# Kernel tuning notes

Measured on AMD Instinct MI355X. Metric: run time of the kernel, lower is better.

Reference implementation:

```python
import jax, jax.numpy as jnp
import numpy as np

KH = KW = 9
BN_EPS = 1e-5


def conv3x3(x, w):
    # x: [B,Cin,H,W], w: [Cout,Cin,3,3], stride 1, padding 1
    return jax.lax.conv_general_dilated(
        x, w, window_strides=(1, 1), padding=((1, 1), (1, 1)),
        dimension_numbers=("NCHW", "OIHW", "NCHW"))


def cbr(x, w, bn):
    # bn: [4, C] rows = (gamma, beta, running_mean, running_var); inference-mode BN
    g, b, m, v = bn[0], bn[1], bn[2], bn[3]
    x = conv3x3(x, w)
    x = (x - m[:, None, None]) * (g[:, None, None] / jnp.sqrt(v[:, None, None] + BN_EPS)) + b[:, None, None]
    return jax.nn.relu(x)


def weighting(x, atten):
    # x: [B,C,H,W], atten: [B,H,W,KH*KW]
    # out[b,c,h,w] = sum_k atten[b,h,w,k] * x[b,c, h+dh(k), w+dw(k)]  (zero-padded window)
    B, C, H, W = x.shape
    patches = jax.lax.conv_general_dilated_patches(
        x, filter_shape=(KH, KW), window_strides=(1, 1),
        padding=((KH // 2, KH // 2), (KW // 2, KW // 2)))  # [B, C*KH*KW, H, W], channel-major
    patches = patches.reshape(B, C, KH * KW, H, W)
    return jnp.einsum("bckhw,bhwk->bchw", patches, atten)


def _make_params(key, fc_dim=1024):
    d4, d16 = fc_dim // 4, fc_dim // 16
    ks = jax.random.split(key, 16)
    def conv_w(k, co, ci):
        return jax.random.normal(k, (co, ci, 3, 3), jnp.float32) * (1.0 / np.sqrt(ci * 9))
    def bn(k, c):
        g = 1.0 + 0.1 * jax.random.normal(k, (c,), jnp.float32)
        return jnp.stack([g, jnp.zeros((c,)), jnp.zeros((c,)), jnp.ones((c,))])
    p = {}
    p["w1"], p["bn1"] = conv_w(ks[0], d4, fc_dim), bn(ks[1], d4)
    p["w2"], p["bn2"] = conv_w(ks[2], d16, d4), bn(ks[3], d16)
    p["w3"], p["bn3"] = conv_w(ks[4], d4, d16), bn(ks[5], d4)
    p["w4"], p["bn4"] = conv_w(ks[6], d4, fc_dim), bn(ks[7], d4)
    p["w5"], p["bn5"] = conv_w(ks[8], d4, d4), bn(ks[9], d4)
    p["fw1"] = jax.random.normal(ks[10], (10, d4), jnp.float32) * (1.0 / np.sqrt(d4))
    p["fb1"] = jnp.zeros((10,), jnp.float32)
    p["fw2"] = jax.random.normal(ks[11], (1, 10), jnp.float32) * (1.0 / np.sqrt(10))
    p["fb2"] = jnp.zeros((1,), jnp.float32)
    return p


def setup_inputs() -> dict:
    key = jax.random.key(0)
    k1, k2, k3, kp = jax.random.split(key, 4)
    B, fc_dim, H, W = 4, 1024, 64, 64
    inp = {
        "low_key": jax.random.normal(k1, (B, fc_dim, H, W), jnp.float32),
        "low_nonkey": jax.random.normal(k2, (B, fc_dim, H, W), jnp.float32),
        "local_atten": jax.random.uniform(k3, (B, H, W, KH * KW), jnp.float32),
    }
    inp.update(_make_params(kp, fc_dim))
    return inp


def reference(low_key, low_nonkey, local_atten,
              w1, bn1, w2, bn2, w3, bn3, w4, bn4, w5, bn5,
              fw1, fb1, fw2, fb2):
    x = cbr(low_key, w1, bn1)        # [B, 256, H, W]
    x = cbr(x, w2, bn2)              # [B, 64, H, W]
    x = weighting(x, local_atten)    # 9x9 local-attention weighted gather
    x = cbr(x, w3, bn3)              # [B, 256, H, W]
    y = cbr(low_nonkey, w4, bn4)     # [B, 256, H, W]
    out = cbr(x - y, w5, bn5)        # [B, 256, H, W]
    out = out.mean(axis=(2, 3))      # adaptive avg pool to 1x1 -> [B, 256]
    out = out @ fw1.T + fb1          # [B, 10]
    out = out @ fw2.T + fb2          # [B, 1]
    return out
```

## Files before the change

### kernel.cpp

```cpp
#include <hip/hip_runtime.h>
#include <math.h>

typedef _Float16 f16;
typedef f16 f16x4 __attribute__((ext_vector_type(4)));
typedef f16 f16x8 __attribute__((ext_vector_type(8)));
typedef float f32x4 __attribute__((ext_vector_type(4)));

#define NB 4

__global__ void __launch_bounds__(256)
wtrans_kernel(const float* __restrict__ w, f16* __restrict__ wt, int Co, int Cin) {
  int idx = blockIdx.x * 256 + threadIdx.x;
  int total = Co * Cin * 9;
  if (idx >= total) return;
  int ci = idx % Cin, t2 = idx / Cin;
  int co = t2 % Co, k = t2 / Co;
  wt[idx] = (f16)w[((size_t)co * Cin + ci) * 9 + k];
}

__global__ void __launch_bounds__(256)
nchw2nhwc(const float* __restrict__ in, f16* __restrict__ out) {
  __shared__ f16 s[64][66];
  const int t = threadIdx.x;
  const int bh = blockIdx.x, c0 = blockIdx.y * 64;
  const int b = bh >> 6, h = bh & 63;
  const int w = t & 63, cr = t >> 6;
  #pragma unroll
  for (int i = 0; i < 16; ++i) {
    int c = c0 + cr * 16 + i;
    s[cr * 16 + i][w] = (f16)in[(((size_t)b * 1024 + c) * 64 + h) * 64 + w];
  }
  __syncthreads();
  #pragma unroll
  for (int i = 0; i < 2; ++i) {
    int task = t + 256 * i;
    int oct = task & 7, w2 = task >> 3;
    f16x8 v;
    #pragma unroll
    for (int j = 0; j < 8; ++j) v[j] = s[oct * 8 + j][w2];
    *(f16x8*)(out + (((size_t)b * 64 + h) * 64 + w2) * 1024 + c0 + oct * 8) = v;
  }
}

__global__ void __launch_bounds__(256, 2)
conv_bigK(const f16* __restrict__ in, const f16* __restrict__ wt,
          float* __restrict__ pacc) {
  constexpr int Cin = 1024, Co = 256, NC = 8;
  __shared__ __align__(16) f16 xs[4][66][40];

  const int t = threadIdx.x;
  const int zz = blockIdx.x;
  const int tile = blockIdx.y;
  const int b = tile >> 5;
  const int h0 = (tile & 31) * 2;
  const int ciBase = zz * 256;
  const int wid = t >> 6, lane = t & 63;
  const int l15 = lane & 15, lg = lane >> 4;
  const int koff = lg * 8;

  f32x4 acc[4][8];
  #pragma unroll
  for (int m = 0; m < 4; ++m)
    #pragma unroll
    for (int n = 0; n < 8; ++n)
      #pragma unroll
      for (int r = 0; r < 4; ++r) acc[m][n][r] = 0.f;

  const f16* inb = in + (size_t)b * Cin * 4096;
  const int wS = t >> 2, octS = t & 3;
  f16x8 ireg[4];

  auto load_stage = [&](int c) {
    int ci0 = ciBase + c * 32;
    #pragma unroll
    for (int r = 0; r < 4; ++r) {
      int gh = h0 - 1 + r;
      f16x8 v = {};
      if ((unsigned)gh < 64u)
        v = *(const f16x8*)(inb + ((size_t)gh * 64 + wS) * Cin + ci0 + octS * 8);
      ireg[r] = v;
    }
  };
  auto write_stage = [&]() {
    #pragma unroll
    for (int r = 0; r < 4; ++r)
      *(f16x8*)&xs[r][wS + 1][octS * 8] = ireg[r];
  };

  const f16* wA = wt + (size_t)(wid * 64 + l15) * Cin + koff + ciBase;

  f16x8 af[3][4];
  #pragma unroll
  for (int m = 0; m < 4; ++m) {
    af[0][m] = *(const f16x8*)(wA + (size_t)m * 16 * Cin);
    af[1][m] = *(const f16x8*)(wA + ((size_t)1 * Co + m * 16) * Cin);
  }

  if (t < 32) {
    int r = t >> 3, side = (t >> 2) & 1, oc = t & 3;
    f16x8 z = {};
    *(f16x8*)&xs[r][side * 65][oc * 8] = z;
  }
  load_stage(0);
  write_stage();
  __syncthreads();

  for (int c = 0; c < NC; ++c) {
    if (c + 1 < NC) load_stage(c + 1);
    #pragma unroll
    for (int tap = 0; tap < 9; ++tap) {
      const int dh = tap / 3 - 1, dw = tap % 3 - 1;
      const int pf_tap = (tap < 7) ? tap + 2 : tap - 7;
      const int pf_c = (tap < 7) ? c : c + 1;
      const bool doPf = (tap < 7) || (c + 1 < NC);
      if (doPf)
        #pragma unroll
        for (int m = 0; m < 4; ++m)
          af[(tap + 2) % 3][m] =
              *(const f16x8*)(wA + ((size_t)pf_tap * Co + m * 16) * Cin + pf_c * 32);
      #pragma unroll
      for (int n = 0; n < 8; ++n) {
        const f16x8 bf = *(const f16x8*)&xs[(n >> 2) + dh + 1][(n & 3) * 16 + l15 + 1 + dw][koff];
        #pragma unroll
        for (int m = 0; m < 4; ++m)
          acc[m][n] = __builtin_amdgcn_mfma_f32_16x16x32_f16(af[tap % 3][m], bf, acc[m][n], 0, 0, 0);
      }
    }
    __syncthreads();
    if (c + 1 < NC) write_stage();
    __syncthreads();
  }

  float* pb = pacc + (size_t)zz * 4194304 + (size_t)b * 4096 * Co;
  #pragma unroll
  for (int m = 0; m < 4; ++m)
    #pragma unroll
    for (int n = 0; n < 8; ++n) {
      int px = (h0 + (n >> 2)) * 64 + (n & 3) * 16 + l15;
      *(f32x4*)(pb + (size_t)px * Co + wid * 64 + m * 16 + lg * 4) = acc[m][n];
    }
}

__global__ void __launch_bounds__(256, 1)
conv_mfma(const f16* __restrict__ in, const f16* __restrict__ in2,
          const f16* __restrict__ wt, const float* __restrict__ bn,
          f16* __restrict__ out, float* __restrict__ pacc,
          float* __restrict__ partial, int Cin, int Co, int kspl) {
  __shared__ __align__(16) f16 xs[6][66][40];
  __shared__ __align__(16) f16 ws[9][64][40];
  __shared__ float s_red[4][64];

  const int t = threadIdx.x;
  const int tile = blockIdx.x;
  const int b = tile >> 4;
  const int h0 = (tile & 15) * 4;
  const int co_blk = blockIdx.y * 64;
  const int ciBase = blockIdx.z * (Cin / kspl);
  const int NC = (Cin / kspl) >> 5;
  const int wid = t >> 6, lane = t & 63;
  const int l15 = lane & 15, lg = lane >> 4;
  const int koff = lg * 8;

  f32x4 acc[4][4];
  #pragma unroll
  for (int m = 0; m < 4; ++m)
    #pragma unroll
    for (int n = 0; n < 4; ++n)
      #pragma unroll
      for (int r = 0; r < 4; ++r) acc[m][n][r] = 0.f;

  const f16* inb = in + (size_t)b * Cin * 4096;
  const f16* inb2 = in2 ? in2 + (size_t)b * Cin * 4096 : nullptr;

  const int wS = t >> 2, octS = t & 3;
  f16x8 ireg[6], wreg[9];

  auto load_stage = [&](int ci0) {
    #pragma unroll
    for (int r = 0; r < 6; ++r) {
      int gh = h0 - 1 + r;
      f16x8 v = {};
      if ((unsigned)gh < 64u) {
        size_t off = ((size_t)gh * 64 + wS) * Cin + ci0 + octS * 8;
        v = *(const f16x8*)(inb + off);
        if (inb2) { f16x8 v2 = *(const f16x8*)(inb2 + off); v = v - v2; }
      }
      ireg[r] = v;
    }
    #pragma unroll
    for (int i = 0; i < 9; ++i) {
      int s = t + 256 * i;
      int oct = s & 3, co = (s >> 2) & 63, k = s >> 8;
      wreg[i] = *(const f16x8*)(wt + ((size_t)k * Co + co_blk + co) * Cin + ci0 + oct * 8);
    }
  };
  auto write_stage = [&]() {
    #pragma unroll
    for (int r = 0; r < 6; ++r)
      *(f16x8*)&xs[r][wS + 1][octS * 8] = ireg[r];
    #pragma unroll
    for (int i = 0; i < 9; ++i) {
      int s = t + 256 * i;
      int oct = s & 3, co = (s >> 2) & 63, k = s >> 8;
      *(f16x8*)&ws[k][co][oct * 8] = wreg[i];
    }
  };

  if (t < 48) {
    int r = t >> 3, side = (t >> 2) & 1, oc = t & 3;
    f16x8 z = {};
    *(f16x8*)&xs[r][side * 65][oc * 8] = z;
  }
  load_stage(ciBase);
  write_stage();
  __syncthreads();

  for (int c = 0; c < NC; ++c) {
    if (c + 1 < NC) load_stage(ciBase + ((c + 1) << 5));
    #pragma unroll
    for (int tap = 0; tap < 9; ++tap) {
      const int dh = tap / 3 - 1, dw = tap % 3 - 1;
      f16x8 af[4];
      #pragma unroll
      for (int m = 0; m < 4; ++m)
        af[m] = *(const f16x8*)&ws[tap][m * 16 + l15][koff];
      #pragma unroll
      for (int n = 0; n < 4; ++n) {
        const f16x8 bf = *(const f16x8*)&xs[wid + dh + 1][n * 16 + l15 + 1 + dw][koff];
        #pragma unroll
        for (int m = 0; m < 4; ++m)
          acc[m][n] = __builtin_amdgcn_mfma_f32_16x16x32_f16(af[m], bf, acc[m][n], 0, 0, 0);
      }
    }
    __syncthreads();
    if (c + 1 < NC) write_stage();
    __syncthreads();
  }

  if (pacc) {
    float* pb = pacc + (size_t)blockIdx.z * 16384 * Co + (size_t)b * 4096 * Co;
    #pragma unroll
    for (int m = 0; m < 4; ++m)
      #pragma unroll
      for (int n = 0; n < 4; ++n) {
        int px = (h0 + wid) * 64 + n * 16 + l15;
        *(f32x4*)(pb + (size_t)px * Co + co_blk + m * 16 + lg * 4) = acc[m][n];
      }
  } else if (out) {
    #pragma unroll
    for (int m = 0; m < 4; ++m) {
      float sc[4], sh[4];
      #pragma unroll
      for (int reg = 0; reg < 4; ++reg) {
        int co = co_blk + m * 16 + lg * 4 + reg;
        sc[reg] = bn[co] / sqrtf(bn[3 * Co + co] + 1e-5f);
        sh[reg] = bn[Co + co] - bn[2 * Co + co] * sc[reg];
      }
      #pragma unroll
      for (int n = 0; n < 4; ++n) {
        f16x4 v;
        #pragma unroll
        for (int reg = 0; reg < 4; ++reg)
          v[reg] = (f16)fmaxf(fmaf(acc[m][n][reg], sc[reg], sh[reg]), 0.f);
        *(f16x4*)(out + ((size_t)(b * 64 + h0 + wid) * 64 + n * 16 + l15) * Co
                      + co_blk + m * 16 + lg * 4) = v;
      }
    }
  } else {
    #pragma unroll
    for (int m = 0; m < 4; ++m)
      #pragma unroll
      for (int reg = 0; reg < 4; ++reg) {
        int co = co_blk + m * 16 + lg * 4 + reg;
        float sc = bn[co] / sqrtf(bn[3 * Co + co] + 1e-5f);
        float sh = bn[Co + co] - bn[2 * Co + co] * sc;
        float s = 0.f;
        #pragma unroll
        for (int n = 0; n < 4; ++n)
          s += fmaxf(fmaf(acc[m][n][reg], sc, sh), 0.f);
        s += __shfl_xor(s, 1, 64);
        s += __shfl_xor(s, 2, 64);
        s += __shfl_xor(s, 4, 64);
        s += __shfl_xor(s, 8, 64);
        if (l15 == 0) s_red[wid][m * 16 + lg * 4 + reg] = s;
      }
    __syncthreads();
    if (t < 64) {
      float v = s_red[0][t] + s_red[1][t] + s_red[2][t] + s_red[3][t];
      partial[((size_t)b * Co + co_blk + t) * 16 + (tile & 15)] = v;
    }
  }
}

__global__ void __launch_bounds__(256)
kreduce(const float* __restrict__ pacc, const float* __restrict__ bn,
        f16* __restrict__ out, int Co, int nslab) {
  const int t = threadIdx.x;
  const size_t slab = (size_t)16384 * Co;
  const int cq = t % (Co >> 2);
  float sc[4], sh[4];
  #pragma unroll
  for (int r = 0; r < 4; ++r) {
    int co = cq * 4 + r;
    sc[r] = bn[co] / sqrtf(bn[3 * Co + co] + 1e-5f);
    sh[r] = bn[Co + co] - bn[2 * Co + co] * sc[r];
  }
  #pragma unroll
  for (int i = 0; i < 4; ++i) {
    size_t idx = (size_t)blockIdx.x * 1024 + i * 256 + t;
    f32x4 a = *(const f32x4*)(pacc + idx * 4);
    for (int s = 1; s < nslab; ++s) {
      f32x4 b2 = *(const f32x4*)(pacc + slab * s + idx * 4);
      #pragma unroll
      for (int r = 0; r < 4; ++r) a[r] += b2[r];
    }
    f16x4 v;
    #pragma unroll
    for (int r = 0; r < 4; ++r)
      v[r] = (f16)fmaxf(fmaf(a[r], sc[r], sh[r]), 0.f);
    *(f16x4*)(out + idx * 4) = v;
  }
}

__global__ void __launch_bounds__(256)
weighting_nhwc(const f16* __restrict__ x, const float* __restrict__ atten,
               f16* __restrict__ out) {
  __shared__ float s_a[64 * 81];
  const int h = blockIdx.x, b = blockIdx.y;
  const int t = threadIdx.x;
  for (int idx = t; idx < 64 * 81; idx += 256)
    s_a[idx] = atten[(size_t)((b * 64 + h) * 64) * 81 + idx];
  __syncthreads();

  const int w = t & 63, cg = t >> 6;
  float acc[16];
  #pragma unroll
  for (int j = 0; j < 16; ++j) acc[j] = 0.f;

  for (int dh = -4; dh <= 4; ++dh) {
    int hh = h + dh;
    if ((unsigned)hh >= 64u) continue;
    #pragma unroll
    for (int dw = -4; dw <= 4; ++dw) {
      int ww = w + dw;
      if ((unsigned)ww >= 64u) continue;
      float a = s_a[w * 81 + (dh + 4) * 9 + (dw + 4)];
      const f16* xp = x + (((size_t)b * 64 + hh) * 64 + ww) * 64 + cg * 16;
      f16x8 v0 = *(const f16x8*)xp;
      f16x8 v1 = *(const f16x8*)(xp + 8);
      #pragma unroll
      for (int j = 0; j < 8; ++j) {
        acc[j]     = fmaf(a, (float)v0[j], acc[j]);
        acc[8 + j] = fmaf(a, (float)v1[j], acc[8 + j]);
      }
    }
  }
  f16x8 o0, o1;
  #pragma unroll
  for (int j = 0; j < 8; ++j) { o0[j] = (f16)acc[j]; o1[j] = (f16)acc[8 + j]; }
  f16* op = out + (((size_t)b * 64 + h) * 64 + w) * 64 + cg * 16;
  *(f16x8*)op = o0;
  *(f16x8*)(op + 8) = o1;
}

__global__ void __launch_bounds__(256)
fc_kernel(const float* __restrict__ partial, const float* __restrict__ fw1,
          const float* __restrict__ fb1, const float* __restrict__ fw2,
          const float* __restrict__ fb2, float* __restrict__ outp) {
  const int t = threadIdx.x;
  const int b = t >> 6, lane = t & 63;
  float pooled[4];
  #pragma unroll
  for (int k = 0; k < 4; ++k) {
    int c = lane + 64 * k;
    float s = 0.f;
    #pragma unroll
    for (int p = 0; p < 16; ++p) s += partial[(size_t)(b * 256 + c) * 16 + p];
    pooled[k] = s * (1.f / 4096.f);
  }
  float o = 0.f;
  for (int i = 0; i < 10; ++i) {
    float d = 0.f;
    #pragma unroll
    for (int k = 0; k < 4; ++k) d += pooled[k] * fw1[i * 256 + lane + 64 * k];
    #pragma unroll
    for (int off = 32; off > 0; off >>= 1) d += __shfl_down(d, off, 64);
    o += (d + fb1[i]) * fw2[i];
  }
  if (lane == 0) outp[b] = o + fb2[0];
}

extern "C" void kernel_launch(void* const* d_in, const int* in_sizes, int n_in,
                              void* d_out, int out_size, void* d_ws, size_t ws_size,
                              hipStream_t stream) {
  const float* low_key    = (const float*)d_in[0];
  const float* low_nonkey = (const float*)d_in[1];
  const float* atten      = (const float*)d_in[2];
  const float* w1 = (const float*)d_in[3];  const float* bn1 = (const float*)d_in[4];
  const float* w2 = (const float*)d_in[5];  const float* bn2 = (const float*)d_in[6];
  const float* w3 = (const float*)d_in[7];  const float* bn3 = (const float*)d_in[8];
  const float* w4 = (const float*)d_in[9];  const float* bn4 = (const float*)d_in[10];
  const float* w5 = (const float*)d_in[11]; const float* bn5 = (const float*)d_in[12];
  const float* fw1 = (const float*)d_in[13]; const float* fb1 = (const float*)d_in[14];
  const float* fw2 = (const float*)d_in[15]; const float* fb2 = (const float*)d_in[16];

  f16* T    = (f16*)d_ws;
  f16* X1   = T + 16777216;
  f16* Y    = X1 + 4194304;
  f16* wt1  = Y + 4194304;
  f16* wt2  = wt1 + 2359296;
  f16* wt3  = wt2 + 147456;
  f16* wt4  = wt3 + 147456;
  f16* wt5  = wt4 + 2359296;
  float* P    = (float*)(wt5 + 589824);
  float* Pacc = P + 16384;
  f16* X2     = (f16*)Pacc;
  f16* X3     = X2 + 1048576;
  float* Pacc2 = Pacc + 2097152;

  dim3 blk(256);
  wtrans_kernel<<<(256 * 1024 * 9 + 255) / 256, blk, 0, stream>>>(w1, wt1, 256, 1024);
  wtrans_kernel<<<(64 * 256 * 9 + 255) / 256, blk, 0, stream>>>(w2, wt2, 64, 256);
  wtrans_kernel<<<(256 * 64 * 9 + 255) / 256, blk, 0, stream>>>(w3, wt3, 256, 64);
  wtrans_kernel<<<(256 * 1024 * 9 + 255) / 256, blk, 0, stream>>>(w4, wt4, 256, 1024);
  wtrans_kernel<<<(256 * 256 * 9 + 255) / 256, blk, 0, stream>>>(w5, wt5, 256, 256);

  nchw2nhwc<<<dim3(256, 16), blk, 0, stream>>>(low_key, T);
  conv_bigK<<<dim3(4, 128, 1), blk, 0, stream>>>(T, wt1, Pacc);
  kreduce<<<1024, blk, 0, stream>>>(Pacc, bn1, X1, 256, 4);
  conv_mfma<<<dim3(64, 1, 4), blk, 0, stream>>>(X1, nullptr, wt2, bn2, nullptr, Pacc2, nullptr, 256, 64, 4);
  kreduce<<<256, blk, 0, stream>>>(Pacc2, bn2, X2, 64, 4);
  weighting_nhwc<<<dim3(64, NB), blk, 0, stream>>>(X2, atten, X3);
  conv_mfma<<<dim3(64, 4, 1), blk, 0, stream>>>(X3, nullptr, wt3, bn3, X1, nullptr, nullptr, 64, 256, 1);
  nchw2nhwc<<<dim3(256, 16), blk, 0, stream>>>(low_nonkey, T);
  conv_bigK<<<dim3(4, 128, 1), blk, 0, stream>>>(T, wt4, Pacc);
  kreduce<<<1024, blk, 0, stream>>>(Pacc, bn4, Y, 256, 4);
  conv_mfma<<<dim3(64, 4, 1), blk, 0, stream>>>(X1, Y, wt5, bn5, nullptr, nullptr, P, 256, 256, 1);
  fc_kernel<<<1, 256, 0, stream>>>(P, fw1, fb1, fw2, fb2, (float*)d_out);
}
```

Before: 396.1 us.

## Replace split-K big conv with direct-to-LDS double-buffered conv and fused BN-ReLU

The two 1024-channel 3x3 convolutions drop the 4-way K split that wrote fp32 partials and needed a separate reduce kernel. A new kernel loops over all input channels, stages both input rows and a re-laid-out weight tensor straight into double-buffered LDS with global_load_lds, and applies BN+ReLU in its epilogue before writing fp16. The NHWC transpose swizzles channel octets so the LDS reads avoid bank conflicts. In exchange the grid shrinks from 512 to 256 blocks at one block per CU, which may leave the machine underused and lengthen each block's serial K loop.

```diff
diff --git a/kernel.cpp b/kernel.cpp
--- a/kernel.cpp
+++ b/kernel.cpp
@@ -7,6 +7,12 @@
 typedef float f32x4 __attribute__((ext_vector_type(4)));
 
 #define NB 4
+
+__device__ inline void gload_lds16(const void* g, void* l) {
+  __builtin_amdgcn_global_load_lds(
+      (const __attribute__((address_space(1))) void*)g,
+      (__attribute__((address_space(3))) void*)l, 16, 0, 0);
+}
 
 __global__ void __launch_bounds__(256)
 wtrans_kernel(const float* __restrict__ w, f16* __restrict__ wt, int Co, int Cin) {
@@ -19,6 +25,14 @@
 }
 
 __global__ void __launch_bounds__(256)
+wtrans_big(const float* __restrict__ w, f16* __restrict__ wtL) {
+  int idx = blockIdx.x * 256 + threadIdx.x;
+  if (idx >= 2359296) return;
+  int j = idx & 7, co = (idx >> 3) & 255, cig = (idx >> 11) & 127, k = idx >> 18;
+  wtL[idx] = (f16)w[((size_t)co * 1024 + cig * 8 + j) * 9 + k];
+}
+
+__global__ void __launch_bounds__(256)
 nchw2nhwc(const float* __restrict__ in, f16* __restrict__ out) {
   __shared__ f16 s[64][66];
   const int t = threadIdx.x;
@@ -38,107 +52,107 @@
     f16x8 v;
     #pragma unroll
     for (int j = 0; j < 8; ++j) v[j] = s[oct * 8 + j][w2];
-    *(f16x8*)(out + (((size_t)b * 64 + h) * 64 + w2) * 1024 + c0 + oct * 8) = v;
-  }
-}
-
-__global__ void __launch_bounds__(256, 2)
-conv_bigK(const f16* __restrict__ in, const f16* __restrict__ wt,
-          float* __restrict__ pacc) {
-  constexpr int Cin = 1024, Co = 256, NC = 8;
-  __shared__ __align__(16) f16 xs[4][66][40];
-
-  const int t = threadIdx.x;
-  const int zz = blockIdx.x;
+    int sw = ((w2 + 1) >> 1) & 3;
+    int po = (oct & 4) | ((oct & 3) ^ sw);
+    *(f16x8*)(out + (((size_t)b * 64 + h) * 64 + w2) * 1024 + c0 + po * 8) = v;
+  }
+}
+
+__global__ void __launch_bounds__(256, 1)
+conv_big2(const f16* __restrict__ in, const f16* __restrict__ wtL,
+          const float* __restrict__ bn, f16* __restrict__ out) {
+  constexpr int Cin = 1024, Co = 256, NC = 32;
+  __shared__ __align__(16) f16 xs[2][6][66][32];
+  __shared__ __align__(16) f16 ws[2][9][4][64][8];
+
+  const int t = threadIdx.x;
+  const int cog = blockIdx.x;
   const int tile = blockIdx.y;
-  const int b = tile >> 5;
-  const int h0 = (tile & 31) * 2;
-  const int ciBase = zz * 256;
+  const int b = tile >> 4;
+  const int h0 = (tile & 15) * 4;
+  const int co_blk = cog * 64;
   const int wid = t >> 6, lane = t & 63;
   const int l15 = lane & 15, lg = lane >> 4;
-  const int koff = lg * 8;
-
-  f32x4 acc[4][8];
+
+  f32x4 acc[4][4];
   #pragma unroll
   for (int m = 0; m < 4; ++m)
     #pragma unroll
-    for (int n = 0; n < 8; ++n)
+    for (int n = 0; n < 4; ++n)
       #pragma unroll
       for (int r = 0; r < 4; ++r) acc[m][n][r] = 0.f;
 
   const f16* inb = in + (size_t)b * Cin * 4096;
-  const int wS = t >> 2, octS = t & 3;
-  f16x8 ireg[4];
-
-  auto load_stage = [&](int c) {
-    int ci0 = ciBase + c * 32;
-    #pragma unroll
-    for (int r = 0; r < 4; ++r) {
+
+  {
+    f16x8 z = {};
+    for (int i = t; i < 3168; i += 256) *(f16x8*)((f16*)xs + (size_t)i * 8) = z;
+  }
+
+  const int wq = wid;
+  const int wS = wq * 16 + (lane >> 2);
+  const int octS = lane & 3;
+
+  auto stage = [&](int c, int bu) {
+    #pragma unroll
+    for (int r = 0; r < 6; ++r) {
       int gh = h0 - 1 + r;
-      f16x8 v = {};
       if ((unsigned)gh < 64u)
-        v = *(const f16x8*)(inb + ((size_t)gh * 64 + wS) * Cin + ci0 + octS * 8);
-      ireg[r] = v;
-    }
+        gload_lds16(inb + ((size_t)gh * 64 + wS) * Cin + c * 32 + octS * 8,
+                    &xs[bu][r][1 + wq * 16][0]);
+    }
+    #pragma unroll
+    for (int k = 0; k < 9; ++k)
+      gload_lds16(wtL + (((size_t)k * 128 + c * 4 + wq) * 256 + co_blk + lane) * 8,
+                  &ws[bu][k][wq][0][0]);
   };
-  auto write_stage = [&]() {
-    #pragma unroll
-    for (int r = 0; r < 4; ++r)
-      *(f16x8*)&xs[r][wS + 1][octS * 8] = ireg[r];
-  };
-
-  const f16* wA = wt + (size_t)(wid * 64 + l15) * Cin + koff + ciBase;
-
-  f16x8 af[3][4];
-  #pragma unroll
-  for (int m = 0; m < 4; ++m) {
-    af[0][m] = *(const f16x8*)(wA + (size_t)m * 16 * Cin);
-    af[1][m] = *(const f16x8*)(wA + ((size_t)1 * Co + m * 16) * Cin);
-  }
-
-  if (t < 32) {
-    int r = t >> 3, side = (t >> 2) & 1, oc = t & 3;
-    f16x8 z = {};
-    *(f16x8*)&xs[r][side * 65][oc * 8] = z;
-  }
-  load_stage(0);
-  write_stage();
+
   __syncthreads();
+  stage(0, 0);
+  __syncthreads();
 
   for (int c = 0; c < NC; ++c) {
-    if (c + 1 < NC) load_stage(c + 1);
+    const int bu = c & 1;
+    if (c + 1 < NC) stage(c + 1, bu ^ 1);
     #pragma unroll
     for (int tap = 0; tap < 9; ++tap) {
       const int dh = tap / 3 - 1, dw = tap % 3 - 1;
-      const int pf_tap = (tap < 7) ? tap + 2 : tap - 7;
-      const int pf_c = (tap < 7) ? c : c + 1;
-      const bool doPf = (tap < 7) || (c + 1 < NC);
-      if (doPf)
+      f16x8 af[4];
+      #pragma unroll
+      for (int m = 0; m < 4; ++m)
+        af[m] = *(const f16x8*)&ws[bu][tap][lg][m * 16 + l15][0];
+      #pragma unroll
+      for (int n = 0; n < 4; ++n) {
+        const int col = n * 16 + l15 + 1 + dw;
+        const int u = lg ^ ((col >> 1) & 3);
+        const f16x8 bf = *(const f16x8*)&xs[bu][wid + dh + 1][col][u * 8];
         #pragma unroll
         for (int m = 0; m < 4; ++m)
-          af[(tap + 2) % 3][m] =
-              *(const f16x8*)(wA + ((size_t)pf_tap * Co + m * 16) * Cin + pf_c * 32);
-      #pragma unroll
-      for (int n = 0; n < 8; ++n) {
-        const f16x8 bf = *(const f16x8*)&xs[(n >> 2) + dh + 1][(n & 3) * 16 + l15 + 1 + dw][koff];
-        #pragma unroll
-        for (int m = 0; m < 4; ++m)
-          acc[m][n] = __builtin_amdgcn_mfma_f32_16x16x32_f16(af[tap % 3][m], bf, acc[m][n], 0, 0, 0);
+          acc[m][n] = __builtin_amdgcn_mfma_f32_16x16x32_f16(af[m], bf, acc[m][n], 0, 0, 0);
       }
     }
     __syncthreads();
-    if (c + 1 < NC) write_stage();
-    __syncthreads();
-  }
-
-  float* pb = pacc + (size_t)zz * 4194304 + (size_t)b * 4096 * Co;
-  #pragma unroll
-  for (int m = 0; m < 4; ++m)
-    #pragma unroll
-    for (int n = 0; n < 8; ++n) {
-      int px = (h0 + (n >> 2)) * 64 + (n & 3) * 16 + l15;
-      *(f32x4*)(pb + (size_t)px * Co + wid * 64 + m * 16 + lg * 4) = acc[m][n];
-    }
+  }
+
+  #pragma unroll
+  for (int m = 0; m < 4; ++m) {
+    float sc[4], sh[4];
+    #pragma unroll
+    for (int reg = 0; reg < 4; ++reg) {
+      int co = co_blk + m * 16 + lg * 4 + reg;
+      sc[reg] = bn[co] / sqrtf(bn[3 * Co + co] + 1e-5f);
+      sh[reg] = bn[Co + co] - bn[2 * Co + co] * sc[reg];
+    }
+    #pragma unroll
+    for (int n = 0; n < 4; ++n) {
+      f16x4 v;
+      #pragma unroll
+      for (int reg = 0; reg < 4; ++reg)
+        v[reg] = (f16)fmaxf(fmaf(acc[m][n][reg], sc[reg], sh[reg]), 0.f);
+      *(f16x4*)(out + ((size_t)(b * 64 + h0 + wid) * 64 + n * 16 + l15) * Co
+                    + co_blk + m * 16 + lg * 4) = v;
+    }
+  }
 }
 
 __global__ void __launch_bounds__(256, 1)
@@ -419,22 +433,20 @@
   float* Pacc2 = Pacc + 2097152;
 
   dim3 blk(256);
-  wtrans_kernel<<<(256 * 1024 * 9 + 255) / 256, blk, 0, stream>>>(w1, wt1, 256, 1024);
+  wtrans_big<<<9216, blk, 0, stream>>>(w1, wt1);
   wtrans_kernel<<<(64 * 256 * 9 + 255) / 256, blk, 0, stream>>>(w2, wt2, 64, 256);
   wtrans_kernel<<<(256 * 64 * 9 + 255) / 256, blk, 0, stream>>>(w3, wt3, 256, 64);
-  wtrans_kernel<<<(256 * 1024 * 9 + 255) / 256, blk, 0, stream>>>(w4, wt4, 256, 1024);
+  wtrans_big<<<9216, blk, 0, stream>>>(w4, wt4);
   wtrans_kernel<<<(256 * 256 * 9 + 255) / 256, blk, 0, stream>>>(w5, wt5, 256, 256);
 
   nchw2nhwc<<<dim3(256, 16), blk, 0, stream>>>(low_key, T);
-  conv_bigK<<<dim3(4, 128, 1), blk, 0, stream>>>(T, wt1, Pacc);
-  kreduce<<<1024, blk, 0, stream>>>(Pacc, bn1, X1, 256, 4);
+  conv_big2<<<dim3(4, 64), blk, 0, stream>>>(T, wt1, bn1, X1);
   conv_mfma<<<dim3(64, 1, 4), blk, 0, stream>>>(X1, nullptr, wt2, bn2, nullptr, Pacc2, nullptr, 256, 64, 4);
   kreduce<<<256, blk, 0, stream>>>(Pacc2, bn2, X2, 64, 4);
   weighting_nhwc<<<dim3(64, NB), blk, 0, stream>>>(X2, atten, X3);
   conv_mfma<<<dim3(64, 4, 1), blk, 0, stream>>>(X3, nullptr, wt3, bn3, X1, nullptr, nullptr, 64, 256, 1);
   nchw2nhwc<<<dim3(256, 16), blk, 0, stream>>>(low_nonkey, T);
-  conv_bigK<<<dim3(4, 128, 1), blk, 0, stream>>>(T, wt4, Pacc);
-  kreduce<<<1024, blk, 0, stream>>>(Pacc, bn4, Y, 256, 4);
+  conv_big2<<<dim3(4, 64), blk, 0, stream>>>(T, wt4, bn4, Y);
   conv_mfma<<<dim3(64, 4, 1), blk, 0, stream>>>(X1, Y, wt5, bn5, nullptr, nullptr, P, 256, 256, 1);
   fc_kernel<<<1, 256, 0, stream>>>(P, fw1, fb1, fw2, fb2, (float*)d_out);
 }
```

After: 349.7 us. -11.7%, faster.
